# Optimization experiments

Hardware: AMD Instinct MI355X
Metric: run time of the kernel (lower is better)

## Reference

```python
import jax, jax.numpy as jnp
import numpy as np


def _log_g(x):
    # log of g(x) = x + 0.5 for x >= 0, sigmoid(x) for x < 0
    return jnp.where(x >= 0, jnp.log(jax.nn.relu(x) + 0.5), -jax.nn.softplus(-x))


def setup_inputs() -> dict:
    key = jax.random.key(0)
    k1, k2 = jax.random.split(key)
    B, S, D = 4, 4096, 1024
    x = jax.random.normal(k1, (B, S, D), dtype=jnp.float32)
    # torch Linear(dim, 2*dim, bias=False) weight layout: [out, in]
    W = jax.random.normal(k2, (2 * D, D), dtype=jnp.float32) * (1.0 / np.sqrt(D))
    return {"x": x, "W": W}


def reference(x, W):
    # x: [B, S, D], W: [2D, D]
    hg = jnp.einsum('bsd,ed->bse', x, W)            # [B, S, 2D]
    hidden, gate = jnp.split(hg, 2, axis=-1)        # each [B, S, D]

    log_coeffs = -jax.nn.softplus(gate)             # log(1 - sigmoid(gate))
    log_z = -jax.nn.softplus(-gate)                 # log(sigmoid(gate))
    log_values = log_z + _log_g(hidden)

    # Heinsen associative scan in log space over the sequence axis
    a_star = jnp.cumsum(log_coeffs, axis=1)
    log_h = a_star + jax.lax.cumlogsumexp(log_values - a_star, axis=1)
    out = jnp.exp(log_h)                            # [B, S, D]; to_out is Identity
    return out
```

## Files before the change

### kernel.cpp

```cpp
#include <hip/hip_runtime.h>
#include <hip/hip_bf16.h>
#include <hip/hip_fp16.h>
#include <cstdint>

typedef unsigned short us;
typedef us   us8 __attribute__((ext_vector_type(8)));
typedef short s8v __attribute__((ext_vector_type(8)));
typedef float f4v __attribute__((ext_vector_type(4)));
typedef __fp16 pk2 __attribute__((ext_vector_type(2)));

#define BB 4
#define SS 4096
#define DD 1024
#define MM (BB * SS)
#define NN (2 * DD)
#define KK DD

#define BM 128
#define BN 128
#define BK 64

#define CHUNK 32
#define NC (SS / CHUNK)
#define BDD (BB * DD)
#define DP (DD / 2)

__device__ inline us f2bf(float f) {
  unsigned u = __float_as_uint(f);
  u += 0x7fffu + ((u >> 16) & 1u);
  return (us)(u >> 16);
}

__global__ __launch_bounds__(256) void cvt_both(const float* __restrict__ x,
                                                const float* __restrict__ W,
                                                us* __restrict__ xb,
                                                us* __restrict__ wb,
                                                long nx) {
  long i = ((long)blockIdx.x * 256 + threadIdx.x) * 8;
  const float* in;
  us* out;
  if (i < nx) { in = x + i; out = xb + i; }
  else        { in = W + (i - nx); out = wb + (i - nx); }
  const float4* p = (const float4*)in;
  float4 a = p[0], b = p[1];
  us8 o;
  o[0] = f2bf(a.x); o[1] = f2bf(a.y); o[2] = f2bf(a.z); o[3] = f2bf(a.w);
  o[4] = f2bf(b.x); o[5] = f2bf(b.y); o[6] = f2bf(b.z); o[7] = f2bf(b.w);
  *(us8*)out = o;
}

#define GLD16(g, l)                                                        \
  __builtin_amdgcn_global_load_lds(                                        \
      (const __attribute__((address_space(1))) void*)(g),                  \
      (__attribute__((address_space(3))) void*)(l), 16, 0, 0)

__device__ inline void gate_cv(float hid, float gat, float& coef, float& v) {
  float e = __expf(gat);
  coef = __builtin_amdgcn_rcpf(1.0f + e);
  float z = 1.0f - coef;
  float eh = __expf(hid < 0.0f ? hid : 0.0f);
  float gneg = eh * __builtin_amdgcn_rcpf(1.0f + eh);
  float g = (hid >= 0.0f) ? (hid + 0.5f) : gneg;
  v = z * g;
}

__global__ __launch_bounds__(256) void gemm_fused(const us* __restrict__ A,
                                                  const us* __restrict__ B,
                                                  unsigned* __restrict__ cv,
                                                  float* __restrict__ cp,
                                                  float* __restrict__ ch) {
  __shared__ __align__(16) us smem[BM * BK + BN * BK];
  us* As = smem;
  us* Bs = smem + BM * BK;
  unsigned* T = (unsigned*)smem;

  const int tid  = threadIdx.x;
  const int lane = tid & 63;
  const int w    = tid >> 6;
  const int wm   = w & 1;
  const int wn   = w >> 1;
  const long bm  = (long)blockIdx.x * BM;
  const int  d0  = blockIdx.y * 64;

  const int srow = lane >> 3;
  const int sseg = (lane & 7) ^ srow;

  const int fr = lane & 15;
  const int fq = lane >> 4;

  int aoff[4][2], boff[4][2];
#pragma unroll
  for (int mt = 0; mt < 4; ++mt) {
    int row = wm * 64 + mt * 16 + fr;
#pragma unroll
    for (int kk = 0; kk < 2; ++kk) {
      int seg = kk * 4 + fq;
      aoff[mt][kk] = row * BK + ((seg ^ (row & 7)) * 8);
    }
  }
#pragma unroll
  for (int nt = 0; nt < 4; ++nt) {
    int row = wn * 64 + nt * 16 + fr;
#pragma unroll
    for (int kk = 0; kk < 2; ++kk) {
      int seg = kk * 4 + fq;
      boff[nt][kk] = row * BK + ((seg ^ (row & 7)) * 8);
    }
  }

  f4v acc[4][4] = {};

  const us* Ap[4];
  const us* Bp[4];
#pragma unroll
  for (int i = 0; i < 4; ++i) {
    int lr = w * 32 + i * 8 + srow;
    Ap[i] = A + (bm + lr) * (long)KK + sseg * 8;
    int wrow = d0 + ((lr >> 5) << 4) + (lr & 15) + (((lr >> 4) & 1) << 10);
    Bp[i] = B + (long)wrow * KK + sseg * 8;
  }

  for (int kt = 0; kt < KK / BK; ++kt) {
    __syncthreads();
#pragma unroll
    for (int i = 0; i < 4; ++i) {
      GLD16(Ap[i], &As[(w * 32 + i * 8) * BK]);
      GLD16(Bp[i], &Bs[(w * 32 + i * 8) * BK]);
      Ap[i] += BK;
      Bp[i] += BK;
    }
    __syncthreads();

#pragma unroll
    for (int kk = 0; kk < 2; ++kk) {
      s8v af[4], bf[4];
#pragma unroll
      for (int mt = 0; mt < 4; ++mt) af[mt] = *(const s8v*)&As[aoff[mt][kk]];
#pragma unroll
      for (int nt = 0; nt < 4; ++nt) bf[nt] = *(const s8v*)&Bs[boff[nt][kk]];
#pragma unroll
      for (int mt = 0; mt < 4; ++mt)
#pragma unroll
        for (int nt = 0; nt < 4; ++nt)
          acc[mt][nt] = __builtin_amdgcn_mfma_f32_16x16x32_bf16(
              af[mt], bf[nt], acc[mt][nt], 0, 0, 0);
    }
  }

  __syncthreads();
#pragma unroll
  for (int mt = 0; mt < 4; ++mt) {
    int lr0 = wm * 64 + mt * 16 + fq * 4;
#pragma unroll
    for (int p = 0; p < 2; ++p) {
      int ld = (wn * 2 + p) * 16 + fr;
      f4v hv = acc[mt][2 * p];
      f4v gv = acc[mt][2 * p + 1];
#pragma unroll
      for (int r = 0; r < 4; ++r) {
        float coef, v;
        gate_cv(hv[r], gv[r], coef, v);
        pk2 pk = __builtin_amdgcn_cvt_pkrtz(coef, v);
        T[(lr0 + r) * 64 + ld] = __builtin_bit_cast(unsigned, pk);
      }
    }
  }
  __syncthreads();

#pragma unroll
  for (int j = 0; j < 8; ++j) {
    int chunk = j * 256 + tid;
    int row = chunk >> 4;
    int q   = chunk & 15;
    uint4 val = *(const uint4*)&T[row * 64 + q * 4];
    *(uint4*)(cv + (size_t)(bm + row) * DD + d0 + q * 4) = val;
  }

  {
    const int d = tid & 63;
    const int c = tid >> 6;
    float P = 1.0f, h = 0.0f;
#pragma unroll
    for (int i = 0; i < CHUNK; ++i) {
      unsigned u = T[(c * CHUNK + i) * 64 + d];
      __half2 hv = *(__half2*)&u;
      float cf = __half2float(hv.x);
      h = fmaf(cf, h, __half2float(hv.y));
      P *= cf;
    }
    const int b  = (int)(bm / SS);
    const int cg = (int)((bm % SS) / CHUNK) + c;
    const int idx = cg * BDD + b * DD + d0 + d;
    cp[idx] = P;
    ch[idx] = h;
  }
}

__global__ __launch_bounds__(256) void scan_pass2(const float* __restrict__ cp,
                                                  const float* __restrict__ ch,
                                                  float* __restrict__ carry) {
  const int bd = blockIdx.x * 256 + threadIdx.x;
  float h = 0.0f;
  for (int c = 0; c < NC; ++c) {
    carry[c * BDD + bd] = h;
    h = fmaf(cp[c * BDD + bd], h, ch[c * BDD + bd]);
  }
}

__global__ __launch_bounds__(256) void scan_pass3(const uint2* __restrict__ cv,
                                                  const float* __restrict__ carry,
                                                  float2* __restrict__ out) {
  const int dp = blockIdx.x * 256 + threadIdx.x;
  const int c = blockIdx.y;
  const int b = blockIdx.z;
  const uint2* base = cv + ((size_t)b * SS + (size_t)c * CHUNK) * DP + dp;
  float2* obase = out + ((size_t)b * SS + (size_t)c * CHUNK) * DP + dp;
  float2 hc = *(const float2*)&carry[c * BDD + b * DD + 2 * dp];
  float h0 = hc.x, h1 = hc.y;
#pragma unroll 8
  for (int t = 0; t < CHUNK; ++t) {
    uint2 u = base[(size_t)t * DP];
    __half2 a = *(__half2*)&u.x;
    __half2 bq = *(__half2*)&u.y;
    h0 = fmaf(__half2float(a.x), h0, __half2float(a.y));
    h1 = fmaf(__half2float(bq.x), h1, __half2float(bq.y));
    obase[(size_t)t * DP] = make_float2(h0, h1);
  }
}

extern "C" void kernel_launch(void* const* d_in, const int* in_sizes, int n_in,
                              void* d_out, int out_size, void* d_ws, size_t ws_size,
                              hipStream_t stream) {
  const float* x = (const float*)d_in[0];
  const float* W = (const float*)d_in[1];
  float2* out = (float2*)d_out;

  const long nx = (long)MM * KK;
  const long nw = (long)NN * KK;

  char* ws = (char*)d_ws;
  unsigned* cv = (unsigned*)ws;      ws += (size_t)MM * DD * sizeof(unsigned);
  us* xb = (us*)ws;                  ws += (size_t)nx * sizeof(us);
  us* wb = (us*)ws;                  ws += (size_t)nw * sizeof(us);
  float* cp = (float*)ws;            ws += (size_t)NC * BDD * sizeof(float);
  float* chh = (float*)ws;           ws += (size_t)NC * BDD * sizeof(float);
  float* carry = (float*)ws;         ws += (size_t)NC * BDD * sizeof(float);

  cvt_both<<<(int)((nx + nw) / 8 / 256), 256, 0, stream>>>(x, W, xb, wb, nx);

  gemm_fused<<<dim3(MM / BM, DD / 64), 256, 0, stream>>>(xb, wb, cv, cp, chh);

  scan_pass2<<<dim3(BDD / 256), 256, 0, stream>>>(cp, chh, carry);
  scan_pass3<<<dim3(DP / 256, NC, BB), 256, 0, stream>>>((const uint2*)cv, carry, out);
}
```

Baseline: 234.2 us.

## Fuse carry scan into output pass with redundant per-chunk prefix recompute

Removes the serial scan_pass2 kernel and its carry buffer. Each output block now rebuilds its own incoming carry by folding all earlier chunk summaries (P,h), so the work grows quadratically in chunk count but needs one fewer launch and no serial 128-step pass with little parallelism. The output pass also moves from float2 to float4 vectorization, with one block per (chunk, batch) covering all of D. The risk is the extra redundant reads of cp/ch for late chunks, and fewer threads per block row.

```diff
diff --git a/kernel.cpp b/kernel.cpp
--- a/kernel.cpp
+++ b/kernel.cpp
@@ -23,7 +23,6 @@
 #define CHUNK 32
 #define NC (SS / CHUNK)
 #define BDD (BB * DD)
-#define DP (DD / 2)
 
 __device__ inline us f2bf(float f) {
   unsigned u = __float_as_uint(f);
@@ -196,35 +195,40 @@
   }
 }
 
-__global__ __launch_bounds__(256) void scan_pass2(const float* __restrict__ cp,
-                                                  const float* __restrict__ ch,
-                                                  float* __restrict__ carry) {
-  const int bd = blockIdx.x * 256 + threadIdx.x;
-  float h = 0.0f;
-  for (int c = 0; c < NC; ++c) {
-    carry[c * BDD + bd] = h;
-    h = fmaf(cp[c * BDD + bd], h, ch[c * BDD + bd]);
-  }
-}
-
-__global__ __launch_bounds__(256) void scan_pass3(const uint2* __restrict__ cv,
-                                                  const float* __restrict__ carry,
-                                                  float2* __restrict__ out) {
-  const int dp = blockIdx.x * 256 + threadIdx.x;
-  const int c = blockIdx.y;
-  const int b = blockIdx.z;
-  const uint2* base = cv + ((size_t)b * SS + (size_t)c * CHUNK) * DP + dp;
-  float2* obase = out + ((size_t)b * SS + (size_t)c * CHUNK) * DP + dp;
-  float2 hc = *(const float2*)&carry[c * BDD + b * DD + 2 * dp];
-  float h0 = hc.x, h1 = hc.y;
+__global__ __launch_bounds__(256) void scan_out(const uint4* __restrict__ cv4,
+                                                const float4* __restrict__ cp4,
+                                                const float4* __restrict__ ch4,
+                                                float4* __restrict__ out4) {
+  const int t4 = threadIdx.x;
+  const int c = blockIdx.x;
+  const int b = blockIdx.y;
+
+  float4 h = make_float4(0.f, 0.f, 0.f, 0.f);
+  for (int j = 0; j < c; ++j) {
+    const int idx = j * (BDD / 4) + b * (DD / 4) + t4;
+    float4 P = cp4[idx];
+    float4 H = ch4[idx];
+    h.x = fmaf(P.x, h.x, H.x);
+    h.y = fmaf(P.y, h.y, H.y);
+    h.z = fmaf(P.z, h.z, H.z);
+    h.w = fmaf(P.w, h.w, H.w);
+  }
+
+  const size_t row0 = (size_t)b * SS + (size_t)c * CHUNK;
+  const uint4* base = cv4 + row0 * (DD / 4) + t4;
+  float4* obase = out4 + row0 * (DD / 4) + t4;
 #pragma unroll 8
   for (int t = 0; t < CHUNK; ++t) {
-    uint2 u = base[(size_t)t * DP];
-    __half2 a = *(__half2*)&u.x;
-    __half2 bq = *(__half2*)&u.y;
-    h0 = fmaf(__half2float(a.x), h0, __half2float(a.y));
-    h1 = fmaf(__half2float(bq.x), h1, __half2float(bq.y));
-    obase[(size_t)t * DP] = make_float2(h0, h1);
+    uint4 u = base[(size_t)t * (DD / 4)];
+    __half2 p0 = *(__half2*)&u.x;
+    __half2 p1 = *(__half2*)&u.y;
+    __half2 p2 = *(__half2*)&u.z;
+    __half2 p3 = *(__half2*)&u.w;
+    h.x = fmaf(__half2float(p0.x), h.x, __half2float(p0.y));
+    h.y = fmaf(__half2float(p1.x), h.y, __half2float(p1.y));
+    h.z = fmaf(__half2float(p2.x), h.z, __half2float(p2.y));
+    h.w = fmaf(__half2float(p3.x), h.w, __half2float(p3.y));
+    obase[(size_t)t * (DD / 4)] = h;
   }
 }
 
@@ -233,7 +237,7 @@
                               hipStream_t stream) {
   const float* x = (const float*)d_in[0];
   const float* W = (const float*)d_in[1];
-  float2* out = (float2*)d_out;
+  float4* out = (float4*)d_out;
 
   const long nx = (long)MM * KK;
   const long nw = (long)NN * KK;
@@ -244,12 +248,12 @@
   us* wb = (us*)ws;                  ws += (size_t)nw * sizeof(us);
   float* cp = (float*)ws;            ws += (size_t)NC * BDD * sizeof(float);
   float* chh = (float*)ws;           ws += (size_t)NC * BDD * sizeof(float);
-  float* carry = (float*)ws;         ws += (size_t)NC * BDD * sizeof(float);
 
   cvt_both<<<(int)((nx + nw) / 8 / 256), 256, 0, stream>>>(x, W, xb, wb, nx);
 
   gemm_fused<<<dim3(MM / BM, DD / 64), 256, 0, stream>>>(xb, wb, cv, cp, chh);
 
-  scan_pass2<<<dim3(BDD / 256), 256, 0, stream>>>(cp, chh, carry);
-  scan_pass3<<<dim3(DP / 256, NC, BB), 256, 0, stream>>>((const uint2*)cv, carry, out);
-}
+  scan_out<<<dim3(NC, BB), 256, 0, stream>>>((const uint4*)cv,
+                                             (const float4*)cp,
+                                             (const float4*)chh, out);
+}
```

Result: slower. 250.1 us (+6.8%).

## Fuse fp32-to-bf16 conversion of x into GEMM A-tile loading

Applied to the files above, without the earlier changes.

Removes the separate pass that converts x to bf16 in workspace; the GEMM now loads fp32 x rows directly into registers, converts with a cheaper rounding, and writes swizzled bf16 into shared memory. Only W is still pre-converted. The grid is also swapped so blocks sharing the same x rows are adjacent, which should improve L2 reuse of the now twice-as-large fp32 A reads. This trades a separate write and read of x in bf16 for fp32 global reads, with the conversion done inside the GEMM and no async LDS load for A, so latency hiding may suffer.

```diff
diff --git a/kernel.cpp b/kernel.cpp
--- a/kernel.cpp
+++ b/kernel.cpp
@@ -30,23 +30,19 @@
   u += 0x7fffu + ((u >> 16) & 1u);
   return (us)(u >> 16);
 }
-
-__global__ __launch_bounds__(256) void cvt_both(const float* __restrict__ x,
-                                                const float* __restrict__ W,
-                                                us* __restrict__ xb,
-                                                us* __restrict__ wb,
-                                                long nx) {
+__device__ inline us f2bf_fast(float f) {
+  return (us)((__float_as_uint(f) + 0x8000u) >> 16);
+}
+
+__global__ __launch_bounds__(256) void cvt_w(const float* __restrict__ W,
+                                             us* __restrict__ wb) {
   long i = ((long)blockIdx.x * 256 + threadIdx.x) * 8;
-  const float* in;
-  us* out;
-  if (i < nx) { in = x + i; out = xb + i; }
-  else        { in = W + (i - nx); out = wb + (i - nx); }
-  const float4* p = (const float4*)in;
+  const float4* p = (const float4*)(W + i);
   float4 a = p[0], b = p[1];
   us8 o;
   o[0] = f2bf(a.x); o[1] = f2bf(a.y); o[2] = f2bf(a.z); o[3] = f2bf(a.w);
   o[4] = f2bf(b.x); o[5] = f2bf(b.y); o[6] = f2bf(b.z); o[7] = f2bf(b.w);
-  *(us8*)out = o;
+  *(us8*)(wb + i) = o;
 }
 
 #define GLD16(g, l)                                                        \
@@ -64,7 +60,7 @@
   v = z * g;
 }
 
-__global__ __launch_bounds__(256) void gemm_fused(const us* __restrict__ A,
+__global__ __launch_bounds__(256) void gemm_fused(const float* __restrict__ X,
                                                   const us* __restrict__ B,
                                                   unsigned* __restrict__ cv,
                                                   float* __restrict__ cp,
@@ -79,11 +75,16 @@
   const int w    = tid >> 6;
   const int wm   = w & 1;
   const int wn   = w >> 1;
-  const long bm  = (long)blockIdx.x * BM;
-  const int  d0  = blockIdx.y * 64;
+  const int  d0  = blockIdx.x * 64;
+  const long bm  = (long)blockIdx.y * BM;
 
   const int srow = lane >> 3;
   const int sseg = (lane & 7) ^ srow;
+
+  const int ar = tid >> 1;
+  const int ah = tid & 1;
+  const float* Arow = X + (bm + ar) * (long)KK + ah * 32;
+  us* Asw = &As[ar * BK];
 
   const int fr = lane & 15;
   const int fq = lane >> 4;
@@ -110,24 +111,35 @@
 
   f4v acc[4][4] = {};
 
-  const us* Ap[4];
   const us* Bp[4];
 #pragma unroll
   for (int i = 0; i < 4; ++i) {
     int lr = w * 32 + i * 8 + srow;
-    Ap[i] = A + (bm + lr) * (long)KK + sseg * 8;
     int wrow = d0 + ((lr >> 5) << 4) + (lr & 15) + (((lr >> 4) & 1) << 10);
     Bp[i] = B + (long)wrow * KK + sseg * 8;
   }
 
   for (int kt = 0; kt < KK / BK; ++kt) {
+    float4 f[8];
+    const float4* src = (const float4*)(Arow + kt * 64);
+#pragma unroll
+    for (int j = 0; j < 8; ++j) f[j] = src[j];
+
     __syncthreads();
 #pragma unroll
     for (int i = 0; i < 4; ++i) {
-      GLD16(Ap[i], &As[(w * 32 + i * 8) * BK]);
       GLD16(Bp[i], &Bs[(w * 32 + i * 8) * BK]);
-      Ap[i] += BK;
       Bp[i] += BK;
+    }
+#pragma unroll
+    for (int j = 0; j < 4; ++j) {
+      us8 o;
+      o[0] = f2bf_fast(f[2 * j].x);     o[1] = f2bf_fast(f[2 * j].y);
+      o[2] = f2bf_fast(f[2 * j].z);     o[3] = f2bf_fast(f[2 * j].w);
+      o[4] = f2bf_fast(f[2 * j + 1].x); o[5] = f2bf_fast(f[2 * j + 1].y);
+      o[6] = f2bf_fast(f[2 * j + 1].z); o[7] = f2bf_fast(f[2 * j + 1].w);
+      int slot = (ah * 4 + j) ^ (ar & 7);
+      *(us8*)&Asw[slot * 8] = o;
     }
     __syncthreads();
 
@@ -169,9 +181,9 @@
 
 #pragma unroll
   for (int j = 0; j < 8; ++j) {
-    int chunk = j * 256 + tid;
-    int row = chunk >> 4;
-    int q   = chunk & 15;
+    int g = j * 256 + tid;
+    int row = g >> 4;
+    int q   = g & 15;
     uint4 val = *(const uint4*)&T[row * 64 + q * 4];
     *(uint4*)(cv + (size_t)(bm + row) * DD + d0 + q * 4) = val;
   }
@@ -235,20 +247,18 @@
   const float* W = (const float*)d_in[1];
   float2* out = (float2*)d_out;
 
-  const long nx = (long)MM * KK;
   const long nw = (long)NN * KK;
 
   char* ws = (char*)d_ws;
   unsigned* cv = (unsigned*)ws;      ws += (size_t)MM * DD * sizeof(unsigned);
-  us* xb = (us*)ws;                  ws += (size_t)nx * sizeof(us);
   us* wb = (us*)ws;                  ws += (size_t)nw * sizeof(us);
   float* cp = (float*)ws;            ws += (size_t)NC * BDD * sizeof(float);
   float* chh = (float*)ws;           ws += (size_t)NC * BDD * sizeof(float);
   float* carry = (float*)ws;         ws += (size_t)NC * BDD * sizeof(float);
 
-  cvt_both<<<(int)((nx + nw) / 8 / 256), 256, 0, stream>>>(x, W, xb, wb, nx);
-
-  gemm_fused<<<dim3(MM / BM, DD / 64), 256, 0, stream>>>(xb, wb, cv, cp, chh);
+  cvt_w<<<(int)(nw / 8 / 256), 256, 0, stream>>>(W, wb);
+
+  gemm_fused<<<dim3(DD / 64, MM / BM), 256, 0, stream>>>(x, wb, cv, cp, chh);
 
   scan_pass2<<<dim3(BDD / 256), 256, 0, stream>>>(cp, chh, carry);
   scan_pass3<<<dim3(DP / 256, NC, BB), 256, 0, stream>>>((const uint2*)cv, carry, out);
```

Result: slower. 315.3 us (+34.6%).
